# Kernel tuning notes

Hardware: AMD Instinct MI355X
Metric: run time of the kernel (lower is better)

The kernel has to match this reference:

```python
import jax, jax.numpy as jnp
import numpy as np

B, C, H, W = 8, 320, 64, 64      # query feature map
S_KV, D_KV = 77, 1024            # key/value (text) tokens
HEADS, DIM_HEAD = 8, 64
INNER = HEADS * DIM_HEAD         # 512


def setup_inputs() -> dict:
    key = jax.random.key(0)
    ks = jax.random.split(key, 7)
    return {
        "query": jax.random.normal(ks[0], (B, C, H, W), dtype=jnp.float32),
        "key_value": jax.random.normal(ks[1], (B, S_KV, D_KV), dtype=jnp.float32),
        "Wq": jax.random.normal(ks[2], (C, INNER), dtype=jnp.float32) * (C ** -0.5),
        "Wk": jax.random.normal(ks[3], (D_KV, INNER), dtype=jnp.float32) * (D_KV ** -0.5),
        "Wv": jax.random.normal(ks[4], (D_KV, INNER), dtype=jnp.float32) * (D_KV ** -0.5),
        "Wo": jax.random.normal(ks[5], (INNER, C), dtype=jnp.float32) * (INNER ** -0.5),
        "bo": jnp.zeros((C,), dtype=jnp.float32),
    }


def reference(query, key_value, Wq, Wk, Wv, Wo, bo):
    b, c, h, w = query.shape
    n = h * w
    # [B,C,H,W] -> [B,N,C]
    q_flat = query.reshape(b, c, n).transpose(0, 2, 1)
    # projections, then split heads: [B, S, heads, dim_head]
    q = (q_flat @ Wq).reshape(b, n, HEADS, DIM_HEAD)
    k = (key_value @ Wk).reshape(b, S_KV, HEADS, DIM_HEAD)
    v = (key_value @ Wv).reshape(b, S_KV, HEADS, DIM_HEAD)
    scale = DIM_HEAD ** -0.5
    # attn logits: [B, heads, N, S_kv]
    logits = jnp.einsum('bnhd,bshd->bhns', q, k) * scale
    attn = jax.nn.softmax(logits, axis=-1)
    # weighted values -> merge heads: [B, N, inner]
    out = jnp.einsum('bhns,bshd->bnhd', attn, v).reshape(b, n, INNER)
    out = out @ Wo + bo  # dropout p=0.0 is identity
    # [B,N,C] -> [B,C,H,W]
    return out.transpose(0, 2, 1).reshape(b, c, h, w)
```

## Files before the change

### kernel.cpp

```cpp
#include <hip/hip_runtime.h>
#include <hip/hip_bf16.h>
#include <stdint.h>

#define BB     8
#define CC     320
#define NN     4096
#define SKV    77
#define HEADS  8
#define INNER  512
#define SCALE  0.125f

typedef float f32x4  __attribute__((ext_vector_type(4)));
typedef short bf16x8 __attribute__((ext_vector_type(8)));
typedef short s16x4  __attribute__((ext_vector_type(4)));

static __device__ __forceinline__ short f2bf(float f) {
  unsigned u = __float_as_uint(f);
  return (short)((u + 0x7fffu + ((u >> 16) & 1u)) >> 16);
}

__global__ __launch_bounds__(256) void prep_kernel(
    const float* __restrict__ kv, const float* __restrict__ Wk,
    const float* __restrict__ Wv, const float* __restrict__ Wq,
    const float* __restrict__ Wo, short* __restrict__ kv_bf,
    short* __restrict__ Wk_t, short* __restrict__ Wv_t,
    short* __restrict__ Wq_t, short* __restrict__ Wo_t,
    unsigned* __restrict__ zero_base) {
  __shared__ float T[64 * 65];
  const int blk = blockIdx.x, t = threadIdx.x;
  if (blk < 616) {
    const int base = blk * 1024;
    #pragma unroll
    for (int i = 0; i < 4; ++i) kv_bf[base + i*256 + t] = f2bf(kv[base + i*256 + t]);
    return;
  }
  if (blk >= 952) {
    const int base = (blk - 952) * 1024;
    #pragma unroll
    for (int i = 0; i < 4; ++i) zero_base[base + i*256 + t] = 0u;
    return;
  }
  const float* src; short* dst; int RS, CS, kt, ct; float scl = 1.0f;
  if (blk < 872) {
    const int tile = blk - 616;
    const bool isK = tile < 128;
    const int tt = isK ? tile : tile - 128;
    src = isK ? Wk : Wv; dst = isK ? Wk_t : Wv_t;
    RS = 1024; CS = 512; kt = tt >> 3; ct = tt & 7;
  } else if (blk < 912) {
    const int tt = blk - 872;
    src = Wq; dst = Wq_t; RS = 320; CS = 512; kt = tt >> 3; ct = tt & 7;
    scl = SCALE;
  } else {
    const int tt = blk - 912;
    src = Wo; dst = Wo_t; RS = 512; CS = 320; kt = tt / 5; ct = tt % 5;
  }
  const int cl = t & 63, rb = t >> 6;
  #pragma unroll
  for (int i = 0; i < 16; ++i)
    T[(rb + i*4)*65 + cl] = src[(size_t)(kt*64 + rb + i*4)*CS + ct*64 + cl];
  __syncthreads();
  #pragma unroll
  for (int i = 0; i < 16; ++i) {
    const int nl = rb + i*4;
    dst[(size_t)(ct*64 + nl)*RS + kt*64 + cl] = f2bf(T[cl*65 + nl] * scl);
  }
}

__global__ __launch_bounds__(256) void kvproj_kernel(
    const short* __restrict__ kv_bf, const short* __restrict__ Wk_t,
    const short* __restrict__ Wv_t, short* __restrict__ K_ws,
    short* __restrict__ V_ws) {
  const int t = threadIdx.x, w = t >> 6, lane = t & 63;
  const int l15 = lane & 15, q = lane >> 4;
  const int m0 = (blockIdx.x * 4 + w) * 16;
  const int y = blockIdx.y;
  const bool isK = (y < 8);
  const int h = y & 7;
  const short* __restrict__ Wt = isK ? Wk_t : Wv_t;
  const int arow = (m0 + l15 < 616) ? (m0 + l15) : 615;

  const f32x4 z = {0.f, 0.f, 0.f, 0.f};
  f32x4 acc[4] = {z, z, z, z};
  for (int k0 = 0; k0 < 1024; k0 += 32) {
    const bf16x8 a = *(const bf16x8*)(kv_bf + arow*1024 + k0 + q*8);
    #pragma unroll
    for (int nt = 0; nt < 4; ++nt) {
      const int n = h*64 + nt*16 + l15;
      const bf16x8 bfr = *(const bf16x8*)(Wt + n*1024 + k0 + q*8);
      acc[nt] = __builtin_amdgcn_mfma_f32_16x16x32_bf16(a, bfr, acc[nt], 0, 0, 0);
    }
  }
  #pragma unroll
  for (int nt = 0; nt < 4; ++nt) {
    const int d = nt*16 + l15;
    #pragma unroll
    for (int r = 0; r < 4; ++r) {
      const int row = m0 + q*4 + r;
      if (row < 616) {
        const int b = (int)(((unsigned)row * 54472u) >> 22);
        const int s = row - b*77;
        if (isK) K_ws[((b*8 + h)*80 + s)*64 + d] = f2bf(acc[nt][r]);
        else     V_ws[((b*8 + h)*64 + d)*96 + s] = f2bf(acc[nt][r]);
      }
    }
  }
}

__global__ __launch_bounds__(256, 2) void fused_kernel(
    const float* __restrict__ query, const short* __restrict__ Wq_t,
    const short* __restrict__ K_ws, const short* __restrict__ V_ws,
    const short* __restrict__ Wo_t, const float* __restrict__ bo,
    float* __restrict__ out) {
  const int t = threadIdx.x, w = t >> 6, lane = t & 63;
  const int l15 = lane & 15, q = lane >> 4;
  const int b = blockIdx.x >> 7;
  const int n0 = (blockIdx.x & 127) * 32;

  __shared__ __align__(16) short Q_lds[32 * 520];
  __shared__ __align__(16) short U[13312];

  const f32x4 z = {0.f, 0.f, 0.f, 0.f};

  {
    const float* qb = query + (size_t)b * CC * NN + n0;
    #pragma unroll
    for (int i = 0; i < 10; ++i) {
      const int f = i * 256 + t;
      const int c = f >> 3, n4 = (f & 7) * 4;
      const f32x4 v = *(const f32x4*)(qb + (size_t)c * NN + n4);
      #pragma unroll
      for (int j = 0; j < 4; ++j)
        U[(n4 + j) * 328 + c] = f2bf(v[j]);
    }
  }
  __syncthreads();

  {
    f32x4 acc[2][8];
    #pragma unroll
    for (int mt = 0; mt < 2; ++mt)
      #pragma unroll
      for (int nt = 0; nt < 8; ++nt) acc[mt][nt] = z;

    const short* __restrict__ Wb = Wq_t + (size_t)(w * 128) * 320;
    auto ld1 = [&](int it, bf16x8 (&A)[2], bf16x8 (&B)[8]) {
      const int k0 = it * 32;
      #pragma unroll
      for (int x = 0; x < 2; ++x)
        A[x] = *(const bf16x8*)(U + (x * 16 + l15) * 328 + k0 + q * 8);
      #pragma unroll
      for (int x = 0; x < 8; ++x)
        B[x] = *(const bf16x8*)(Wb + (size_t)(x * 16 + l15) * 320 + k0 + q * 8);
    };
    bf16x8 aP[2], bP[8], aN[2], bN[8];
    ld1(0, aP, bP);
    #pragma unroll
    for (int it = 0; it < 10; ++it) {
      if (it + 1 < 10) ld1(it + 1, aN, bN);
      #pragma unroll
      for (int mt = 0; mt < 2; ++mt)
        #pragma unroll
        for (int nt = 0; nt < 8; ++nt)
          acc[mt][nt] = __builtin_amdgcn_mfma_f32_16x16x32_bf16(aP[mt], bP[nt], acc[mt][nt], 0, 0, 0);
      #pragma unroll
      for (int x = 0; x < 2; ++x) aP[x] = aN[x];
      #pragma unroll
      for (int x = 0; x < 8; ++x) bP[x] = bN[x];
    }
    #pragma unroll
    for (int mt = 0; mt < 2; ++mt)
      #pragma unroll
      for (int r = 0; r < 4; ++r) {
        const int tok = mt * 16 + q * 4 + r;
        #pragma unroll
        for (int nt = 0; nt < 8; ++nt)
          Q_lds[tok * 520 + w * 128 + nt * 16 + l15] = f2bf(acc[mt][nt][r]);
      }
  }
  __syncthreads();

  {
    short* scrw = U + w * 3328;
    for (int i = lane; i < 256; i += 64)
      *(unsigned*)(scrw + (i >> 3) * 104 + 80 + (i & 7) * 2) = 0u;

    #pragma unroll
    for (int hh = 0; hh < 2; ++hh) {
      const int h = w * 2 + hh;
      const short* __restrict__ Kh = K_ws + (size_t)(b * 8 + h) * 80 * 64;
      const short* __restrict__ Vh = V_ws + (size_t)(b * 8 + h) * 64 * 96;

      f32x4 qk[2][5];
      #pragma unroll
      for (int nt = 0; nt < 2; ++nt)
        #pragma unroll
        for (int st = 0; st < 5; ++st) qk[nt][st] = z;
      #pragma unroll
      for (int f = 0; f < 2; ++f) {
        bf16x8 bq[2];
        #pragma unroll
        for (int nt = 0; nt < 2; ++nt)
          bq[nt] = *(const bf16x8*)(Q_lds + (nt * 16 + l15) * 520 + h * 64 + f * 32 + q * 8);
        #pragma unroll
        for (int st = 0; st < 5; ++st) {
          const bf16x8 a = *(const bf16x8*)(Kh + (st * 16 + l15) * 64 + f * 32 + q * 8);
          #pragma unroll
          for (int nt = 0; nt < 2; ++nt)
            qk[nt][st] = __builtin_amdgcn_mfma_f32_16x16x32_bf16(a, bq[nt], qk[nt][st], 0, 0, 0);
        }
      }

      #pragma unroll
      for (int nt = 0; nt < 2; ++nt) {
        float mx = -1e30f;
        #pragma unroll
        for (int st = 0; st < 5; ++st)
          #pragma unroll
          for (int r = 0; r < 4; ++r) {
            const int s = st * 16 + q * 4 + r;
            const float vv = (s < SKV) ? qk[nt][st][r] : -1e30f;
            qk[nt][st][r] = vv;
            mx = fmaxf(mx, vv);
          }
        mx = fmaxf(mx, __shfl_xor(mx, 16));
        mx = fmaxf(mx, __shfl_xor(mx, 32));
        float sum = 0.f;
        #pragma unroll
        for (int st = 0; st < 5; ++st)
          #pragma unroll
          for (int r = 0; r < 4; ++r) {
            const int s = st * 16 + q * 4 + r;
            const float e = (s < SKV) ? __expf(qk[nt][st][r] - mx) : 0.f;
            qk[nt][st][r] = e;
            sum += e;
          }
        sum += __shfl_xor(sum, 16);
        sum += __shfl_xor(sum, 32);
        const float inv = 1.0f / sum;
        #pragma unroll
        for (int st = 0; st < 5; ++st) {
          s16x4 pv;
          #pragma unroll
          for (int r = 0; r < 4; ++r) pv[r] = f2bf(qk[nt][st][r] * inv);
          *(s16x4*)(scrw + (nt * 16 + l15) * 104 + st * 16 + q * 4) = pv;
        }
      }

      f32x4 ov[2][4];
      #pragma unroll
      for (int nt = 0; nt < 2; ++nt)
        #pragma unroll
        for (int dt = 0; dt < 4; ++dt) ov[nt][dt] = z;
      #pragma unroll
      for (int f = 0; f < 3; ++f) {
        bf16x8 bp[2];
        #pragma unroll
        for (int nt = 0; nt < 2; ++nt)
          bp[nt] = *(const bf16x8*)(scrw + (nt * 16 + l15) * 104 + f * 32 + q * 8);
        #pragma unroll
        for (int dt = 0; dt < 4; ++dt) {
          const bf16x8 a = *(const bf16x8*)(Vh + (dt * 16 + l15) * 96 + f * 32 + q * 8);
          #pragma unroll
          for (int nt = 0; nt < 2; ++nt)
            ov[nt][dt] = __builtin_amdgcn_mfma_f32_16x16x32_bf16(a, bp[nt], ov[nt][dt], 0, 0, 0);
        }
      }
      #pragma unroll
      for (int nt = 0; nt < 2; ++nt)
        #pragma unroll
        for (int dt = 0; dt < 4; ++dt) {
          s16x4 pv;
          #pragma unroll
          for (int r = 0; r < 4; ++r) pv[r] = f2bf(ov[nt][dt][r]);
          *(s16x4*)(Q_lds + (nt * 16 + l15) * 520 + h * 64 + dt * 16 + q * 4) = pv;
        }
    }
  }
  __syncthreads();

  {
    f32x4 oc[5][2];
    #pragma unroll
    for (int mt = 0; mt < 5; ++mt)
      #pragma unroll
      for (int nt = 0; nt < 2; ++nt) oc[mt][nt] = z;

    const short* __restrict__ Wa = Wo_t + (size_t)(w * 80) * 512;
    auto ld3 = [&](int it, bf16x8 (&A)[5], bf16x8 (&B)[2]) {
      const int k0 = it * 32;
      #pragma unroll
      for (int x = 0; x < 5; ++x)
        A[x] = *(const bf16x8*)(Wa + (size_t)(x * 16 + l15) * 512 + k0 + q * 8);
      #pragma unroll
      for (int x = 0; x < 2; ++x)
        B[x] = *(const bf16x8*)(Q_lds + (x * 16 + l15) * 520 + k0 + q * 8);
    };
    bf16x8 aP[5], bP[2], aN[5], bN[2];
    ld3(0, aP, bP);
    #pragma unroll
    for (int it = 0; it < 16; ++it) {
      if (it + 1 < 16) ld3(it + 1, aN, bN);
      #pragma unroll
      for (int mt = 0; mt < 5; ++mt)
        #pragma unroll
        for (int nt = 0; nt < 2; ++nt)
          oc[mt][nt] = __builtin_amdgcn_mfma_f32_16x16x32_bf16(aP[mt], bP[nt], oc[mt][nt], 0, 0, 0);
      #pragma unroll
      for (int x = 0; x < 5; ++x) aP[x] = aN[x];
      #pragma unroll
      for (int x = 0; x < 2; ++x) bP[x] = bN[x];
    }
    #pragma unroll
    for (int mt = 0; mt < 5; ++mt)
      #pragma unroll
      for (int r = 0; r < 4; ++r) {
        const int c = w * 80 + mt * 16 + q * 4 + r;
        const float bv = bo[c];
        float* rowp = out + ((size_t)(b * CC + c)) * NN + n0;
        #pragma unroll
        for (int nt = 0; nt < 2; ++nt)
          rowp[nt * 16 + l15] = oc[mt][nt][r] + bv;
      }
  }
}

extern "C" void kernel_launch(void* const* d_in, const int* in_sizes, int n_in,
                              void* d_out, int out_size, void* d_ws, size_t ws_size,
                              hipStream_t stream) {
  const float* query = (const float*)d_in[0];
  const float* kv    = (const float*)d_in[1];
  const float* Wq    = (const float*)d_in[2];
  const float* Wk    = (const float*)d_in[3];
  const float* Wv    = (const float*)d_in[4];
  const float* Wo    = (const float*)d_in[5];
  const float* bo    = (const float*)d_in[6];
  float* out = (float*)d_out;

  char* p = (char*)d_ws;
  short* K_ws  = (short*)(p);
  short* V_ws  = (short*)(p +   819200);
  short* Wq_t  = (short*)(p +  1802240);
  short* Wo_t  = (short*)(p +  2129920);
  short* kv_bf = (short*)(p +  2457600);
  short* Wk_t  = (short*)(p +  3719168);
  short* Wv_t  = (short*)(p +  4767744);

  prep_kernel<<<1192, 256, 0, stream>>>(kv, Wk, Wv, Wq, Wo, kv_bf,
                                        Wk_t, Wv_t, Wq_t, Wo_t,
                                        (unsigned*)V_ws);
  kvproj_kernel<<<dim3(10, 16), 256, 0, stream>>>(kv_bf, Wk_t, Wv_t, K_ws, V_ws);
  fused_kernel<<<1024, 256, 0, stream>>>(query, Wq_t, K_ws, V_ws, Wo_t, bo, out);
}
```

Measured before the change: 211.3 us.

## Double token tile per block and stage weights into swizzled LDS via direct loads

Each fused block now covers 64 query tokens with 512 threads instead of 32 tokens with 256, so each Wq and Wo tile fetched from global memory is reused across twice as many tokens. Wq and Wo tiles are loaded with global_load_lds into double-buffered, XOR-swizzled LDS buffers rather than into per-wave registers, and waves share those tiles. Attention now assigns one head per wave, looping over two 32-token groups. The trade-off is a single large LDS allocation that likely allows only one block per CU, plus a block-wide barrier on every k-step.

```diff
diff --git a/kernel.cpp b/kernel.cpp
--- a/kernel.cpp
+++ b/kernel.cpp
@@ -17,6 +17,14 @@
 static __device__ __forceinline__ short f2bf(float f) {
   unsigned u = __float_as_uint(f);
   return (short)((u + 0x7fffu + ((u >> 16) & 1u)) >> 16);
+}
+
+static __device__ __forceinline__ void gll16(void* lds, const void* g) {
+  auto gp = reinterpret_cast<const uint32_t __attribute__((address_space(1)))*>(
+      reinterpret_cast<uintptr_t>(g));
+  auto lp = reinterpret_cast<uint32_t __attribute__((address_space(3)))*>(
+      reinterpret_cast<uintptr_t>(lds));
+  __builtin_amdgcn_global_load_lds(gp, lp, 16, 0, 0);
 }
 
 __global__ __launch_bounds__(256) void prep_kernel(
@@ -107,18 +115,17 @@
   }
 }
 
-__global__ __launch_bounds__(256, 2) void fused_kernel(
+__global__ __launch_bounds__(512, 2) void fused_kernel(
     const float* __restrict__ query, const short* __restrict__ Wq_t,
     const short* __restrict__ K_ws, const short* __restrict__ V_ws,
     const short* __restrict__ Wo_t, const float* __restrict__ bo,
     float* __restrict__ out) {
   const int t = threadIdx.x, w = t >> 6, lane = t & 63;
   const int l15 = lane & 15, q = lane >> 4;
-  const int b = blockIdx.x >> 7;
-  const int n0 = (blockIdx.x & 127) * 32;
-
-  __shared__ __align__(16) short Q_lds[32 * 520];
-  __shared__ __align__(16) short U[13312];
+  const int b = blockIdx.x >> 6;
+  const int n0 = (blockIdx.x & 63) * 64;
+
+  __shared__ short S[59904];
 
   const f32x4 z = {0.f, 0.f, 0.f, 0.f};
 
@@ -126,71 +133,80 @@
     const float* qb = query + (size_t)b * CC * NN + n0;
     #pragma unroll
     for (int i = 0; i < 10; ++i) {
-      const int f = i * 256 + t;
-      const int c = f >> 3, n4 = (f & 7) * 4;
+      const int f = i * 512 + t;
+      const int c = f >> 4, n4 = (f & 15) * 4;
       const f32x4 v = *(const f32x4*)(qb + (size_t)c * NN + n4);
       #pragma unroll
       for (int j = 0; j < 4; ++j)
-        U[(n4 + j) * 328 + c] = f2bf(v[j]);
-    }
-  }
-  __syncthreads();
+        S[(n4 + j) * 330 + c] = f2bf(v[j]);
+    }
+  }
 
   {
-    f32x4 acc[2][8];
-    #pragma unroll
-    for (int mt = 0; mt < 2; ++mt)
-      #pragma unroll
-      for (int nt = 0; nt < 8; ++nt) acc[mt][nt] = z;
-
-    const short* __restrict__ Wb = Wq_t + (size_t)(w * 128) * 320;
-    auto ld1 = [&](int it, bf16x8 (&A)[2], bf16x8 (&B)[8]) {
+    f32x4 acc[4][4];
+    #pragma unroll
+    for (int mt = 0; mt < 4; ++mt)
+      #pragma unroll
+      for (int nt = 0; nt < 4; ++nt) acc[mt][nt] = z;
+
+    auto stageB = [&](int it, int pbuf) {
       const int k0 = it * 32;
-      #pragma unroll
-      for (int x = 0; x < 2; ++x)
-        A[x] = *(const bf16x8*)(U + (x * 16 + l15) * 328 + k0 + q * 8);
-      #pragma unroll
-      for (int x = 0; x < 8; ++x)
-        B[x] = *(const bf16x8*)(Wb + (size_t)(x * 16 + l15) * 320 + k0 + q * 8);
+      short* dstb = S + 21120 + pbuf * 16384;
+      #pragma unroll
+      for (int p = 0; p < 4; ++p) {
+        const int L = p * 512 + t;
+        const int j = L >> 2, qp = L & 3;
+        const int ql = qp ^ ((j >> 1) & 3);
+        gll16(dstb + L * 8, Wq_t + (size_t)j * 320 + k0 + ql * 8);
+      }
     };
-    bf16x8 aP[2], bP[8], aN[2], bN[8];
-    ld1(0, aP, bP);
-    #pragma unroll
+
+    stageB(0, 0);
+    __syncthreads();
     for (int it = 0; it < 10; ++it) {
-      if (it + 1 < 10) ld1(it + 1, aN, bN);
-      #pragma unroll
-      for (int mt = 0; mt < 2; ++mt)
-        #pragma unroll
-        for (int nt = 0; nt < 8; ++nt)
-          acc[mt][nt] = __builtin_amdgcn_mfma_f32_16x16x32_bf16(aP[mt], bP[nt], acc[mt][nt], 0, 0, 0);
-      #pragma unroll
-      for (int x = 0; x < 2; ++x) aP[x] = aN[x];
-      #pragma unroll
-      for (int x = 0; x < 8; ++x) bP[x] = bN[x];
-    }
-    #pragma unroll
-    for (int mt = 0; mt < 2; ++mt)
+      if (it + 1 < 10) stageB(it + 1, (it + 1) & 1);
+      const int k0 = it * 32;
+      const short* Bb = S + 21120 + (it & 1) * 16384;
+      bf16x8 a[4], bb[4];
+      #pragma unroll
+      for (int mt = 0; mt < 4; ++mt)
+        a[mt] = *(const bf16x8*)(S + (mt * 16 + l15) * 330 + k0 + q * 8);
+      #pragma unroll
+      for (int nt = 0; nt < 4; ++nt) {
+        const int jr = w * 64 + nt * 16 + l15;
+        const int a16 = jr * 4 + (q ^ ((jr >> 1) & 3));
+        bb[nt] = *(const bf16x8*)(Bb + a16 * 8);
+      }
+      #pragma unroll
+      for (int mt = 0; mt < 4; ++mt)
+        #pragma unroll
+        for (int nt = 0; nt < 4; ++nt)
+          acc[mt][nt] = __builtin_amdgcn_mfma_f32_16x16x32_bf16(a[mt], bb[nt], acc[mt][nt], 0, 0, 0);
+      __syncthreads();
+    }
+    #pragma unroll
+    for (int mt = 0; mt < 4; ++mt)
       #pragma unroll
       for (int r = 0; r < 4; ++r) {
         const int tok = mt * 16 + q * 4 + r;
         #pragma unroll
-        for (int nt = 0; nt < 8; ++nt)
-          Q_lds[tok * 520 + w * 128 + nt * 16 + l15] = f2bf(acc[mt][nt][r]);
-      }
-  }
-  __syncthreads();
+        for (int nt = 0; nt < 4; ++nt)
+          S[tok * 520 + w * 64 + nt * 16 + l15] = f2bf(acc[mt][nt][r]);
+      }
+  }
 
   {
-    short* scrw = U + w * 3328;
-    for (int i = lane; i < 256; i += 64)
-      *(unsigned*)(scrw + (i >> 3) * 104 + 80 + (i & 7) * 2) = 0u;
-
-    #pragma unroll
-    for (int hh = 0; hh < 2; ++hh) {
-      const int h = w * 2 + hh;
-      const short* __restrict__ Kh = K_ws + (size_t)(b * 8 + h) * 80 * 64;
-      const short* __restrict__ Vh = V_ws + (size_t)(b * 8 + h) * 64 * 96;
-
+    short* scrw = S + 33280 + w * 3328;
+    #pragma unroll
+    for (int i = 0; i < 4; ++i) {
+      const int f = lane + i * 64;
+      *(unsigned*)(scrw + (f >> 3) * 104 + 80 + (f & 7) * 2) = 0u;
+    }
+    const short* __restrict__ Kh = K_ws + (size_t)(b * 8 + w) * 80 * 64;
+    const short* __restrict__ Vh = V_ws + (size_t)(b * 8 + w) * 64 * 96;
+
+    for (int g = 0; g < 2; ++g) {
+      const int tb = g * 32;
       f32x4 qk[2][5];
       #pragma unroll
       for (int nt = 0; nt < 2; ++nt)
@@ -201,7 +217,7 @@
         bf16x8 bq[2];
         #pragma unroll
         for (int nt = 0; nt < 2; ++nt)
-          bq[nt] = *(const bf16x8*)(Q_lds + (nt * 16 + l15) * 520 + h * 64 + f * 32 + q * 8);
+          bq[nt] = *(const bf16x8*)(S + (tb + nt * 16 + l15) * 520 + w * 64 + f * 32 + q * 8);
         #pragma unroll
         for (int st = 0; st < 5; ++st) {
           const bf16x8 a = *(const bf16x8*)(Kh + (st * 16 + l15) * 64 + f * 32 + q * 8);
@@ -273,51 +289,65 @@
           s16x4 pv;
           #pragma unroll
           for (int r = 0; r < 4; ++r) pv[r] = f2bf(ov[nt][dt][r]);
-          *(s16x4*)(Q_lds + (nt * 16 + l15) * 520 + h * 64 + dt * 16 + q * 4) = pv;
+          *(s16x4*)(S + (tb + nt * 16 + l15) * 520 + w * 64 + dt * 16 + q * 4) = pv;
         }
     }
   }
   __syncthreads();
 
   {
+    const int wm = w & 3;
+    const int wg = w >> 2;
     f32x4 oc[5][2];
     #pragma unroll
     for (int mt = 0; mt < 5; ++mt)
       #pragma unroll
       for (int nt = 0; nt < 2; ++nt) oc[mt][nt] = z;
 
-    const short* __restrict__ Wa = Wo_t + (size_t)(w * 80) * 512;
-    auto ld3 = [&](int it, bf16x8 (&A)[5], bf16x8 (&B)[2]) {
+    auto stageW = [&](int it, int pbuf) {
       const int k0 = it * 32;
-      #pragma unroll
-      for (int x = 0; x < 5; ++x)
-        A[x] = *(const bf16x8*)(Wa + (size_t)(x * 16 + l15) * 512 + k0 + q * 8);
-      #pragma unroll
-      for (int x = 0; x < 2; ++x)
-        B[x] = *(const bf16x8*)(Q_lds + (x * 16 + l15) * 520 + k0 + q * 8);
+      short* dstb = S + 33280 + pbuf * 10240;
+      #pragma unroll
+      for (int p = 0; p < 3; ++p) {
+        const int L = p * 512 + t;
+        if (L < 1280) {
+          const int j = L >> 2, qp = L & 3;
+          const int ql = qp ^ ((j >> 1) & 3);
+          gll16(dstb + L * 8, Wo_t + (size_t)j * 512 + k0 + ql * 8);
+        }
+      }
     };
-    bf16x8 aP[5], bP[2], aN[5], bN[2];
-    ld3(0, aP, bP);
-    #pragma unroll
+
+    stageW(0, 0);
+    __syncthreads();
     for (int it = 0; it < 16; ++it) {
-      if (it + 1 < 16) ld3(it + 1, aN, bN);
+      if (it + 1 < 16) stageW(it + 1, (it + 1) & 1);
+      const int k0 = it * 32;
+      const short* Wb = S + 33280 + (it & 1) * 10240;
+      bf16x8 a[5], bb[2];
+      #pragma unroll
+      for (int mt = 0; mt < 5; ++mt) {
+        const int jr = wm * 80 + mt * 16 + l15;
+        const int a16 = jr * 4 + (q ^ ((jr >> 1) & 3));
+        a[mt] = *(const bf16x8*)(Wb + a16 * 8);
+      }
+      #pragma unroll
+      for (int nt = 0; nt < 2; ++nt)
+        bb[nt] = *(const bf16x8*)(S + (wg * 32 + nt * 16 + l15) * 520 + k0 + q * 8);
       #pragma unroll
       for (int mt = 0; mt < 5; ++mt)
         #pragma unroll
         for (int nt = 0; nt < 2; ++nt)
-          oc[mt][nt] = __builtin_amdgcn_mfma_f32_16x16x32_bf16(aP[mt], bP[nt], oc[mt][nt], 0, 0, 0);
-      #pragma unroll
-      for (int x = 0; x < 5; ++x) aP[x] = aN[x];
-      #pragma unroll
-      for (int x = 0; x < 2; ++x) bP[x] = bN[x];
+          oc[mt][nt] = __builtin_amdgcn_mfma_f32_16x16x32_bf16(a[mt], bb[nt], oc[mt][nt], 0, 0, 0);
+      if (it + 1 < 16) __syncthreads();
     }
     #pragma unroll
     for (int mt = 0; mt < 5; ++mt)
       #pragma unroll
       for (int r = 0; r < 4; ++r) {
-        const int c = w * 80 + mt * 16 + q * 4 + r;
+        const int c = wm * 80 + mt * 16 + q * 4 + r;
         const float bv = bo[c];
-        float* rowp = out + ((size_t)(b * CC + c)) * NN + n0;
+        float* rowp = out + ((size_t)(b * CC + c)) * NN + n0 + wg * 32;
         #pragma unroll
         for (int nt = 0; nt < 2; ++nt)
           rowp[nt * 16 + l15] = oc[mt][nt][r] + bv;
@@ -350,5 +380,5 @@
                                         Wk_t, Wv_t, Wq_t, Wo_t,
                                         (unsigned*)V_ws);
   kvproj_kernel<<<dim3(10, 16), 256, 0, stream>>>(kv_bf, Wk_t, Wv_t, K_ws, V_ws);
-  fused_kernel<<<1024, 256, 0, stream>>>(query, Wq_t, K_ws, V_ws, Wo_t, bo, out);
-}
+  fused_kernel<<<512, 512, 0, stream>>>(query, Wq_t, K_ws, V_ws, Wo_t, bo, out);
+}
```

Measured after the change: 176.8 us. 1.2x faster.

## Stream weight tiles via global_load_lds into per-wave LDS slices, raise occupancy

Applied to the files above, without the earlier changes.

Replaces the register double-buffered weight loads in the Q-projection and output-projection GEMMs with direct global-to-LDS async loads (global_load_lds) into a per-wave slice, synchronised with explicit waitcnt and sched barriers. The two shared arrays are merged into one buffer and the attention stage processes 16 tokens at a time to cut register pressure. Launch bounds go from 2 to 3 blocks per SM. The aim is higher occupancy and less VGPR use. In exchange it takes more LDS traffic and serialises each load behind vmcnt(0) waits, and several block-wide barriers are removed, which risks races on the shared buffer.

```diff
diff --git a/kernel.cpp b/kernel.cpp
--- a/kernel.cpp
+++ b/kernel.cpp
@@ -17,6 +17,14 @@
 static __device__ __forceinline__ short f2bf(float f) {
   unsigned u = __float_as_uint(f);
   return (short)((u + 0x7fffu + ((u >> 16) & 1u)) >> 16);
+}
+
+static __device__ __forceinline__ void gll16(void* lds, const void* g) {
+  auto gp = reinterpret_cast<const uint32_t __attribute__((address_space(1)))*>(
+      reinterpret_cast<uintptr_t>(g));
+  auto lp = reinterpret_cast<uint32_t __attribute__((address_space(3)))*>(
+      reinterpret_cast<uintptr_t>(lds));
+  __builtin_amdgcn_global_load_lds(gp, lp, 16, 0, 0);
 }
 
 __global__ __launch_bounds__(256) void prep_kernel(
@@ -107,7 +115,7 @@
   }
 }
 
-__global__ __launch_bounds__(256, 2) void fused_kernel(
+__global__ __launch_bounds__(256, 3) void fused_kernel(
     const float* __restrict__ query, const short* __restrict__ Wq_t,
     const short* __restrict__ K_ws, const short* __restrict__ V_ws,
     const short* __restrict__ Wo_t, const float* __restrict__ bo,
@@ -117,8 +125,8 @@
   const int b = blockIdx.x >> 7;
   const int n0 = (blockIdx.x & 127) * 32;
 
-  __shared__ __align__(16) short Q_lds[32 * 520];
-  __shared__ __align__(16) short U[13312];
+  __shared__ short S[26880];
+  short* slice = S + 16640 + w * 2560;
 
   const f32x4 z = {0.f, 0.f, 0.f, 0.f};
 
@@ -131,10 +139,9 @@
       const f32x4 v = *(const f32x4*)(qb + (size_t)c * NN + n4);
       #pragma unroll
       for (int j = 0; j < 4; ++j)
-        U[(n4 + j) * 328 + c] = f2bf(v[j]);
-    }
-  }
-  __syncthreads();
+        S[(n4 + j) * 328 + c] = f2bf(v[j]);
+    }
+  }
 
   {
     f32x4 acc[2][8];
@@ -143,31 +150,56 @@
       #pragma unroll
       for (int nt = 0; nt < 8; ++nt) acc[mt][nt] = z;
 
-    const short* __restrict__ Wb = Wq_t + (size_t)(w * 128) * 320;
-    auto ld1 = [&](int it, bf16x8 (&A)[2], bf16x8 (&B)[8]) {
+    const short* __restrict__ Wqw = Wq_t + (size_t)(w * 128) * 320;
+    auto stage1 = [&](int it, int h2) {
       const int k0 = it * 32;
       #pragma unroll
-      for (int x = 0; x < 2; ++x)
-        A[x] = *(const bf16x8*)(U + (x * 16 + l15) * 328 + k0 + q * 8);
-      #pragma unroll
-      for (int x = 0; x < 8; ++x)
-        B[x] = *(const bf16x8*)(Wb + (size_t)(x * 16 + l15) * 320 + k0 + q * 8);
+      for (int p = 0; p < 4; ++p) {
+        const int L = p * 64 + lane;
+        gll16(slice + L * 8,
+              Wqw + (size_t)(h2 * 64 + (L >> 2)) * 320 + k0 + (L & 3) * 8);
+      }
     };
-    bf16x8 aP[2], bP[8], aN[2], bN[8];
-    ld1(0, aP, bP);
-    #pragma unroll
+
+    stage1(0, 0);
+    __syncthreads();
+
     for (int it = 0; it < 10; ++it) {
-      if (it + 1 < 10) ld1(it + 1, aN, bN);
+      const int k0 = it * 32;
+      asm volatile("s_waitcnt vmcnt(0)" ::: "memory");
+      __builtin_amdgcn_sched_barrier(0);
+      bf16x8 a[2], b0[4];
       #pragma unroll
       for (int mt = 0; mt < 2; ++mt)
-        #pragma unroll
-        for (int nt = 0; nt < 8; ++nt)
-          acc[mt][nt] = __builtin_amdgcn_mfma_f32_16x16x32_bf16(aP[mt], bP[nt], acc[mt][nt], 0, 0, 0);
-      #pragma unroll
-      for (int x = 0; x < 2; ++x) aP[x] = aN[x];
-      #pragma unroll
-      for (int x = 0; x < 8; ++x) bP[x] = bN[x];
-    }
+        a[mt] = *(const bf16x8*)(S + (mt * 16 + l15) * 328 + k0 + q * 8);
+      #pragma unroll
+      for (int x = 0; x < 4; ++x)
+        b0[x] = *(const bf16x8*)(slice + (x * 16 + l15) * 32 + q * 8);
+      asm volatile("s_waitcnt lgkmcnt(0)" ::: "memory");
+      __builtin_amdgcn_sched_barrier(0);
+      stage1(it, 1);
+      #pragma unroll
+      for (int mt = 0; mt < 2; ++mt)
+        #pragma unroll
+        for (int x = 0; x < 4; ++x)
+          acc[mt][x] = __builtin_amdgcn_mfma_f32_16x16x32_bf16(a[mt], b0[x], acc[mt][x], 0, 0, 0);
+
+      asm volatile("s_waitcnt vmcnt(0)" ::: "memory");
+      __builtin_amdgcn_sched_barrier(0);
+      bf16x8 b1[4];
+      #pragma unroll
+      for (int x = 0; x < 4; ++x)
+        b1[x] = *(const bf16x8*)(slice + (x * 16 + l15) * 32 + q * 8);
+      asm volatile("s_waitcnt lgkmcnt(0)" ::: "memory");
+      __builtin_amdgcn_sched_barrier(0);
+      if (it + 1 < 10) stage1(it + 1, 0);
+      #pragma unroll
+      for (int mt = 0; mt < 2; ++mt)
+        #pragma unroll
+        for (int x = 0; x < 4; ++x)
+          acc[mt][4 + x] = __builtin_amdgcn_mfma_f32_16x16x32_bf16(a[mt], b1[x], acc[mt][4 + x], 0, 0, 0);
+    }
+    __syncthreads();
     #pragma unroll
     for (int mt = 0; mt < 2; ++mt)
       #pragma unroll
@@ -175,52 +207,44 @@
         const int tok = mt * 16 + q * 4 + r;
         #pragma unroll
         for (int nt = 0; nt < 8; ++nt)
-          Q_lds[tok * 520 + w * 128 + nt * 16 + l15] = f2bf(acc[mt][nt][r]);
-      }
-  }
-  __syncthreads();
+          S[tok * 520 + w * 128 + nt * 16 + l15] = f2bf(acc[mt][nt][r]);
+      }
+  }
 
   {
-    short* scrw = U + w * 3328;
-    for (int i = lane; i < 256; i += 64)
-      *(unsigned*)(scrw + (i >> 3) * 104 + 80 + (i & 7) * 2) = 0u;
-
+    short* scrw = slice;
+    #pragma unroll
+    for (int i = 0; i < 2; ++i) {
+      const int f = i * 64 + lane;
+      *(unsigned*)(scrw + (f >> 3) * 104 + 80 + (f & 7) * 2) = 0u;
+    }
     #pragma unroll
     for (int hh = 0; hh < 2; ++hh) {
-      const int h = w * 2 + hh;
+      const int h = 2 * w + hh;
       const short* __restrict__ Kh = K_ws + (size_t)(b * 8 + h) * 80 * 64;
       const short* __restrict__ Vh = V_ws + (size_t)(b * 8 + h) * 64 * 96;
-
-      f32x4 qk[2][5];
-      #pragma unroll
-      for (int nt = 0; nt < 2; ++nt)
-        #pragma unroll
-        for (int st = 0; st < 5; ++st) qk[nt][st] = z;
-      #pragma unroll
-      for (int f = 0; f < 2; ++f) {
-        bf16x8 bq[2];
-        #pragma unroll
-        for (int nt = 0; nt < 2; ++nt)
-          bq[nt] = *(const bf16x8*)(Q_lds + (nt * 16 + l15) * 520 + h * 64 + f * 32 + q * 8);
-        #pragma unroll
-        for (int st = 0; st < 5; ++st) {
-          const bf16x8 a = *(const bf16x8*)(Kh + (st * 16 + l15) * 64 + f * 32 + q * 8);
-          #pragma unroll
-          for (int nt = 0; nt < 2; ++nt)
-            qk[nt][st] = __builtin_amdgcn_mfma_f32_16x16x32_bf16(a, bq[nt], qk[nt][st], 0, 0, 0);
+      for (int c16 = 0; c16 < 2; ++c16) {
+        const int tb = c16 * 16;
+        f32x4 qk[5];
+        #pragma unroll
+        for (int st = 0; st < 5; ++st) qk[st] = z;
+        #pragma unroll
+        for (int f = 0; f < 2; ++f) {
+          const bf16x8 bq = *(const bf16x8*)(S + (tb + l15) * 520 + h * 64 + f * 32 + q * 8);
+          #pragma unroll
+          for (int st = 0; st < 5; ++st) {
+            const bf16x8 a = *(const bf16x8*)(Kh + (st * 16 + l15) * 64 + f * 32 + q * 8);
+            qk[st] = __builtin_amdgcn_mfma_f32_16x16x32_bf16(a, bq, qk[st], 0, 0, 0);
+          }
         }
-      }
-
-      #pragma unroll
-      for (int nt = 0; nt < 2; ++nt) {
         float mx = -1e30f;
         #pragma unroll
         for (int st = 0; st < 5; ++st)
           #pragma unroll
           for (int r = 0; r < 4; ++r) {
             const int s = st * 16 + q * 4 + r;
-            const float vv = (s < SKV) ? qk[nt][st][r] : -1e30f;
-            qk[nt][st][r] = vv;
+            const float vv = (s < SKV) ? qk[st][r] : -1e30f;
+            qk[st][r] = vv;
             mx = fmaxf(mx, vv);
           }
         mx = fmaxf(mx, __shfl_xor(mx, 16));
@@ -231,8 +255,8 @@
           #pragma unroll
           for (int r = 0; r < 4; ++r) {
             const int s = st * 16 + q * 4 + r;
-            const float e = (s < SKV) ? __expf(qk[nt][st][r] - mx) : 0.f;
-            qk[nt][st][r] = e;
+            const float e = (s < SKV) ? __expf(qk[st][r] - mx) : 0.f;
+            qk[st][r] = e;
             sum += e;
           }
         sum += __shfl_xor(sum, 16);
@@ -242,42 +266,31 @@
         for (int st = 0; st < 5; ++st) {
           s16x4 pv;
           #pragma unroll
-          for (int r = 0; r < 4; ++r) pv[r] = f2bf(qk[nt][st][r] * inv);
-          *(s16x4*)(scrw + (nt * 16 + l15) * 104 + st * 16 + q * 4) = pv;
+          for (int r = 0; r < 4; ++r) pv[r] = f2bf(qk[st][r] * inv);
+          *(s16x4*)(scrw + l15 * 104 + st * 16 + q * 4) = pv;
         }
-      }
-
-      f32x4 ov[2][4];
-      #pragma unroll
-      for (int nt = 0; nt < 2; ++nt)
-        #pragma unroll
-        for (int dt = 0; dt < 4; ++dt) ov[nt][dt] = z;
-      #pragma unroll
-      for (int f = 0; f < 3; ++f) {
-        bf16x8 bp[2];
-        #pragma unroll
-        for (int nt = 0; nt < 2; ++nt)
-          bp[nt] = *(const bf16x8*)(scrw + (nt * 16 + l15) * 104 + f * 32 + q * 8);
-        #pragma unroll
-        for (int dt = 0; dt < 4; ++dt) {
-          const bf16x8 a = *(const bf16x8*)(Vh + (dt * 16 + l15) * 96 + f * 32 + q * 8);
-          #pragma unroll
-          for (int nt = 0; nt < 2; ++nt)
-            ov[nt][dt] = __builtin_amdgcn_mfma_f32_16x16x32_bf16(a, bp[nt], ov[nt][dt], 0, 0, 0);
+        f32x4 ov[4];
+        #pragma unroll
+        for (int dt = 0; dt < 4; ++dt) ov[dt] = z;
+        #pragma unroll
+        for (int f = 0; f < 3; ++f) {
+          const bf16x8 bp = *(const bf16x8*)(scrw + l15 * 104 + f * 32 + q * 8);
+          #pragma unroll
+          for (int dt = 0; dt < 4; ++dt) {
+            const bf16x8 a = *(const bf16x8*)(Vh + (dt * 16 + l15) * 96 + f * 32 + q * 8);
+            ov[dt] = __builtin_amdgcn_mfma_f32_16x16x32_bf16(a, bp, ov[dt], 0, 0, 0);
+          }
         }
-      }
-      #pragma unroll
-      for (int nt = 0; nt < 2; ++nt)
         #pragma unroll
         for (int dt = 0; dt < 4; ++dt) {
           s16x4 pv;
           #pragma unroll
-          for (int r = 0; r < 4; ++r) pv[r] = f2bf(ov[nt][dt][r]);
-          *(s16x4*)(Q_lds + (nt * 16 + l15) * 520 + h * 64 + dt * 16 + q * 4) = pv;
+          for (int r = 0; r < 4; ++r) pv[r] = f2bf(ov[dt][r]);
+          *(s16x4*)(S + (tb + l15) * 520 + h * 64 + dt * 16 + q * 4) = pv;
         }
-    }
-  }
-  __syncthreads();
+      }
+    }
+  }
 
   {
     f32x4 oc[5][2];
@@ -286,30 +299,37 @@
       #pragma unroll
       for (int nt = 0; nt < 2; ++nt) oc[mt][nt] = z;
 
-    const short* __restrict__ Wa = Wo_t + (size_t)(w * 80) * 512;
-    auto ld3 = [&](int it, bf16x8 (&A)[5], bf16x8 (&B)[2]) {
+    const short* __restrict__ Wow = Wo_t + (size_t)(w * 80) * 512;
+    auto stage3 = [&](int it) {
       const int k0 = it * 32;
       #pragma unroll
-      for (int x = 0; x < 5; ++x)
-        A[x] = *(const bf16x8*)(Wa + (size_t)(x * 16 + l15) * 512 + k0 + q * 8);
-      #pragma unroll
-      for (int x = 0; x < 2; ++x)
-        B[x] = *(const bf16x8*)(Q_lds + (x * 16 + l15) * 520 + k0 + q * 8);
+      for (int p = 0; p < 5; ++p) {
+        const int L = p * 64 + lane;
+        gll16(slice + L * 8, Wow + (size_t)(L >> 2) * 512 + k0 + (L & 3) * 8);
+      }
     };
-    bf16x8 aP[5], bP[2], aN[5], bN[2];
-    ld3(0, aP, bP);
-    #pragma unroll
+
+    stage3(0);
+    __syncthreads();
     for (int it = 0; it < 16; ++it) {
-      if (it + 1 < 16) ld3(it + 1, aN, bN);
+      const int k0 = it * 32;
+      asm volatile("s_waitcnt vmcnt(0)" ::: "memory");
+      __builtin_amdgcn_sched_barrier(0);
+      bf16x8 a[5], bb[2];
       #pragma unroll
       for (int mt = 0; mt < 5; ++mt)
+        a[mt] = *(const bf16x8*)(slice + (mt * 16 + l15) * 32 + q * 8);
+      #pragma unroll
+      for (int nt = 0; nt < 2; ++nt)
+        bb[nt] = *(const bf16x8*)(S + (nt * 16 + l15) * 520 + k0 + q * 8);
+      asm volatile("s_waitcnt lgkmcnt(0)" ::: "memory");
+      __builtin_amdgcn_sched_barrier(0);
+      if (it + 1 < 16) stage3(it + 1);
+      #pragma unroll
+      for (int mt = 0; mt < 5; ++mt)
         #pragma unroll
         for (int nt = 0; nt < 2; ++nt)
-          oc[mt][nt] = __builtin_amdgcn_mfma_f32_16x16x32_bf16(aP[mt], bP[nt], oc[mt][nt], 0, 0, 0);
-      #pragma unroll
-      for (int x = 0; x < 5; ++x) aP[x] = aN[x];
-      #pragma unroll
-      for (int x = 0; x < 2; ++x) bP[x] = bN[x];
+          oc[mt][nt] = __builtin_amdgcn_mfma_f32_16x16x32_bf16(a[mt], bb[nt], oc[mt][nt], 0, 0, 0);
     }
     #pragma unroll
     for (int mt = 0; mt < 5; ++mt)
```

After: 182.4 us. 13.7% less time.
